# Kernel tuning notes

Measured on AMD Instinct MI355X. Metric: run time of the kernel, lower is better.

## Reference

```python
import jax, jax.numpy as jnp
import numpy as np

B, R, D, P = 32, 512, 256, 5532  # images, rois/image, feat dim, num_pids
NEG_INF = -1e30

def setup_inputs() -> dict:
    key = jax.random.key(0)
    k1, k2, k3 = jax.random.split(key, 3)
    inputs = jax.random.normal(k1, (B * R, D), dtype=jnp.float32)
    cls_scores = jax.random.uniform(k2, (B * R, 1), dtype=jnp.float32)
    roi_label = jax.random.randint(k3, (B, R), 0, P + 1)  # 0 = background -> label -1
    return {"inputs": inputs, "cls_scores": cls_scores, "roi_label": roi_label}

def reference(inputs, cls_scores, roi_label):
    x = (inputs * cls_scores).reshape(B, R, D)          # scale features by cls score
    label = roi_label - 1                               # [B,R], -1 = background
    valid = label >= 0                                  # keep labeled ROIs only
    lbl = jnp.where(valid, label, 0)

    # per-image per-pid mean prototypes via one segmented reduction
    seg = (jnp.arange(B)[:, None] * P + lbl).reshape(-1)             # [B*R]
    w = valid.reshape(-1).astype(x.dtype)
    sums = jax.ops.segment_sum(x.reshape(-1, D) * w[:, None], seg, num_segments=B * P)
    counts = jax.ops.segment_sum(w, seg, num_segments=B * P)          # [B*P]
    proto = sums / jnp.maximum(counts, 1.0)[:, None]
    proto = proto / jnp.maximum(jnp.linalg.norm(proto, axis=-1, keepdims=True), 1e-12)
    proto = jax.lax.stop_gradient(proto).reshape(B, P, D)            # .detach() in torch
    present = (counts > 0).reshape(B, P)                              # unique labels per image

    # project each ROI feature onto its image's prototypes
    logits = jnp.einsum('brd,bpd->brp', x, proto)                     # [B,R,P]
    logits = jnp.where(present[:, None, :], logits, NEG_INF)          # softmax over unique labels only
    logp = jax.nn.log_softmax(logits, axis=-1)
    nll = -jnp.take_along_axis(logp, lbl[..., None], axis=-1)[..., 0] # [B,R]
    nll = jnp.where(valid, nll, 0.0)
    n_valid = jnp.maximum(jnp.sum(valid).astype(x.dtype), 1.0)
    return jnp.sum(nll) / n_valid
```

## Files before the change

### kernel.cpp

```cpp
#include <hip/hip_runtime.h>
#include <math.h>

#define Bn 32
#define Rn 512
#define Dn 256
#define Pn 5532
#define MAXU 512

#define TRr 32
#define TCc 128
#define KCs 64
#define NSTG (Dn / KCs)
#define NBLK ((Rn / TRr) * Bn)

#define PBF_OFF    0
#define PBF_WORDS  (Bn*MAXU*Dn/2)
#define LBLC_OFF   (PBF_OFF + PBF_WORDS)
#define NUNIQ_OFF  (LBLC_OFF + Bn*Rn)
#define NVALID_OFF (NUNIQ_OFF + 32)
#define NLL_OFF    (NVALID_OFF + 32)
#define TICK_OFF   (NLL_OFF + 1)

typedef short short8 __attribute__((ext_vector_type(8)));
typedef short short4v __attribute__((ext_vector_type(4)));
typedef float floatx4 __attribute__((ext_vector_type(4)));

__device__ __forceinline__ unsigned short bf16r(float f) {
    union { float f; unsigned int u; } c; c.f = f;
    return (unsigned short)((c.u + 0x7FFFu + ((c.u >> 16) & 1u)) >> 16);
}
__device__ __forceinline__ float bfu2f(unsigned int hi16) {
    union { unsigned int u; float f; } c; c.u = hi16;
    return c.f;
}

__device__ __forceinline__ void async16(void* lds, const void* g) {
    auto* l3 = reinterpret_cast<__attribute__((address_space(3))) unsigned int*>(
                   reinterpret_cast<size_t>(lds));
    auto* g1 = reinterpret_cast<const __attribute__((address_space(1))) unsigned int*>(
                   reinterpret_cast<size_t>(g));
    __builtin_amdgcn_global_load_lds(g1, l3, 16, 0, 0);
}

__global__ __launch_bounds__(1024) void k12_prep_proto(
    const float* __restrict__ inputs, const float* __restrict__ cls,
    const int* __restrict__ roi_label,
    unsigned short* __restrict__ pbf, int* __restrict__ lblc_arr,
    int* __restrict__ nuniq, int* __restrict__ nvalid_arr,
    int* __restrict__ zwords)
{
    __shared__ int cnt_lds[Pn];
    __shared__ int cmap_lds[Pn];
    __shared__ int curs_lds[MAXU];
    __shared__ int scnt_lds[MAXU];
    __shared__ int rl_lds[Rn];
    __shared__ int wpres[16], wcnt[16];

    const int b = blockIdx.x;
    const int t = threadIdx.x;
    const int lane = t & 63, wid = t >> 6;

    if (b == 0 && t == 0) { zwords[0] = 0; zwords[1] = 0; }

    for (int i = t; i < Pn; i += 1024) cnt_lds[i] = 0;
    __syncthreads();
    int mylbl = -1;
    if (t < Rn) {
        mylbl = roi_label[b * Rn + t] - 1;
        if (mylbl >= 0) atomicAdd(&cnt_lds[mylbl], 1);
    }
    __syncthreads();

    int basePres = 0, baseCnt = 0;
    for (int i0 = 0; i0 < Pn; i0 += 1024) {
        int i = i0 + t;
        int cnt = (i < Pn) ? cnt_lds[i] : 0;
        bool pres = cnt > 0;
        unsigned long long mask = __ballot(pres);
        int pfx_pres = __popcll(mask & ((1ULL << lane) - 1ULL));
        int v = cnt;
        #pragma unroll
        for (int off = 1; off < 64; off <<= 1) {
            int u = __shfl_up(v, off);
            if (lane >= off) v += u;
        }
        int pfx_cnt = v - cnt;
        if (lane == 63) { wpres[wid] = __popcll(mask); wcnt[wid] = v; }
        __syncthreads();
        int woffP = 0, totP = 0, woffC = 0, totC = 0;
        #pragma unroll
        for (int w = 0; w < 16; ++w) {
            int p = wpres[w], c = wcnt[w];
            if (w < wid) { woffP += p; woffC += c; }
            totP += p; totC += c;
        }
        if (pres) {
            int c = basePres + woffP + pfx_pres;
            cmap_lds[i] = c;
            scnt_lds[c] = cnt;
            curs_lds[c] = baseCnt + woffC + pfx_cnt;
        }
        basePres += totP; baseCnt += totC;
        __syncthreads();
    }
    if (t < Rn) {
        int lc = (mylbl >= 0) ? cmap_lds[mylbl] : -1;
        lblc_arr[b * Rn + t] = lc;
        if (lc >= 0) {
            int pos = atomicAdd(&curs_lds[lc], 1);
            rl_lds[pos] = t;
        }
    }
    if (t == 0) { nuniq[b] = basePres; nvalid_arr[b] = baseCnt; }
    __syncthreads();
    const int U = basePres;

    for (int cb = wid; cb < U; cb += 64) {
        int cntj[4], stj[4];
        #pragma unroll
        for (int j = 0; j < 4; ++j) {
            int c = cb + 16 * j;
            bool ok = c < U;
            int cnt = ok ? scnt_lds[c] : 0;
            cntj[j] = cnt;
            stj[j]  = ok ? (curs_lds[c] - cnt) : 0;
        }
        int rj[4];
        #pragma unroll
        for (int j = 0; j < 4; ++j) rj[j] = cntj[j] ? rl_lds[stj[j]] : 0;
        float cwj[4]; float4 vj[4];
        #pragma unroll
        for (int j = 0; j < 4; ++j) {
            int row = b * Rn + rj[j];
            cwj[j] = cls[row];
            vj[j]  = *(const float4*)&inputs[(size_t)row * Dn + lane * 4];
        }
        #pragma unroll
        for (int j = 0; j < 4; ++j) {
            if (!cntj[j]) continue;
            float a0 = bfu2f(((unsigned)bf16r(vj[j].x * cwj[j])) << 16);
            float a1 = bfu2f(((unsigned)bf16r(vj[j].y * cwj[j])) << 16);
            float a2 = bfu2f(((unsigned)bf16r(vj[j].z * cwj[j])) << 16);
            float a3 = bfu2f(((unsigned)bf16r(vj[j].w * cwj[j])) << 16);
            for (int k = 1; k < cntj[j]; ++k) {
                int row = b * Rn + rl_lds[stj[j] + k];
                float cw = cls[row];
                float4 v = *(const float4*)&inputs[(size_t)row * Dn + lane * 4];
                a0 += bfu2f(((unsigned)bf16r(v.x * cw)) << 16);
                a1 += bfu2f(((unsigned)bf16r(v.y * cw)) << 16);
                a2 += bfu2f(((unsigned)bf16r(v.z * cw)) << 16);
                a3 += bfu2f(((unsigned)bf16r(v.w * cw)) << 16);
            }
            float inv = 1.0f / (float)cntj[j];
            a0 *= inv; a1 *= inv; a2 *= inv; a3 *= inv;
            float ss = a0*a0 + a1*a1 + a2*a2 + a3*a3;
            #pragma unroll
            for (int off = 32; off > 0; off >>= 1) ss += __shfl_xor(ss, off);
            float sc = 1.0f / fmaxf(sqrtf(ss), 1e-12f);
            short4v o;
            o[0] = (short)bf16r(a0 * sc); o[1] = (short)bf16r(a1 * sc);
            o[2] = (short)bf16r(a2 * sc); o[3] = (short)bf16r(a3 * sc);
            int s = b * MAXU + cb + 16 * j;
            *(short4v*)&pbf[(size_t)s * Dn + lane * 4] = o;
        }
    }
}

__global__ __launch_bounds__(256, 2) void k3_loss(
    const float* __restrict__ inputs, const float* __restrict__ cls,
    const unsigned short* __restrict__ pbf,
    const int* __restrict__ lblc_arr, const int* __restrict__ nuniq,
    const int* __restrict__ nvalid_arr,
    float* __restrict__ nll, int* __restrict__ tick, float* __restrict__ out)
{
    __shared__ __align__(16) unsigned short xs[TRr * Dn];
    __shared__ __align__(16) unsigned short psb[2][TCc * KCs];
    __shared__ int lblc[TRr];
    __shared__ float es_l[4][TRr];
    __shared__ float ds_l[4][TRr];

    const int t = threadIdx.x;
    const int lane = t & 63, w = t >> 6;
    const int q = lane >> 4, r15 = lane & 15;
    const int rt = blockIdx.x;
    const int b  = blockIdx.y;
    const int roiBase = rt * TRr;
    const int U = nuniq[b];
    const int nch = (U <= 0) ? 1 : ((U + TCc - 1) >> 7);

    if (t < TRr) lblc[t] = lblc_arr[b * Rn + roiBase + t];

#define ISSUE_PS(PC, ST, BUF)                                                \
    do {                                                                     \
        _Pragma("unroll")                                                    \
        for (int i_ = 0; i_ < 4; ++i_) {                                     \
            int ci_ = i_ * 256 + w * 64 + lane;                              \
            int pr_ = ci_ >> 3, gp_ = ci_ & 7;                               \
            int g_ = gp_ ^ (pr_ & 7);                                        \
            async16(&psb[BUF][(i_ * 256 + w * 64) * 8],                      \
                    pbf + (size_t)(b * MAXU + (PC) * TCc + pr_) * Dn         \
                        + (ST) * KCs + g_ * 8);                              \
        }                                                                    \
    } while (0)

    ISSUE_PS(0, 0, 0);

    {
        const int row = t >> 3, seg = t & 7;
        const size_t gbase = (size_t)(b * Rn + roiBase + row) * Dn + seg * 32;
        const float cw = cls[b * Rn + roiBase + row];
        #pragma unroll
        for (int jj = 0; jj < 4; ++jj) {
            float4 v0 = *(const float4*)&inputs[gbase + jj * 8];
            float4 v1 = *(const float4*)&inputs[gbase + jj * 8 + 4];
            short8 o;
            o[0] = (short)bf16r(v0.x * cw); o[1] = (short)bf16r(v0.y * cw);
            o[2] = (short)bf16r(v0.z * cw); o[3] = (short)bf16r(v0.w * cw);
            o[4] = (short)bf16r(v1.x * cw); o[5] = (short)bf16r(v1.y * cw);
            o[6] = (short)bf16r(v1.z * cw); o[7] = (short)bf16r(v1.w * cw);
            int gpos = (seg * 4 + jj) ^ (row & 7);
            *(short8*)&xs[row * Dn + gpos * 8] = o;
        }
    }
    __syncthreads();

    short8 areg[2][8];
    #pragma unroll
    for (int mt = 0; mt < 2; ++mt)
        #pragma unroll
        for (int kcs = 0; kcs < 8; ++kcs) {
            int row = mt * 16 + r15;
            int gpos = (kcs * 4 + q) ^ (row & 7);
            areg[mt][kcs] = *(const short8*)&xs[row * Dn + gpos * 8];
        }

    int lcr[2][4];
    float esum[2][4], dsum[2][4];
    #pragma unroll
    for (int mt = 0; mt < 2; ++mt)
        #pragma unroll
        for (int reg = 0; reg < 4; ++reg) {
            lcr[mt][reg] = lblc[mt * 16 + q * 4 + reg];
            esum[mt][reg] = 0.f; dsum[mt][reg] = 0.f;
        }

    for (int pc = 0; pc < nch; ++pc) {
        floatx4 acc[2][2];
        #pragma unroll
        for (int mt = 0; mt < 2; ++mt) {
            acc[mt][0] = (floatx4)0.f; acc[mt][1] = (floatx4)0.f;
        }

        #pragma unroll
        for (int st = 0; st < NSTG; ++st) {
            const int cur = st & 1;
            __syncthreads();
            int ns = pc * NSTG + st + 1;
            if (ns < nch * NSTG) ISSUE_PS(ns >> 2, ns & 3, cur ^ 1);
            #pragma unroll
            for (int kk = 0; kk < 2; ++kk) {
                short8 bb[2];
                #pragma unroll
                for (int nt = 0; nt < 2; ++nt) {
                    int r = w * 32 + nt * 16 + r15;
                    int gpos = (kk * 4 + q) ^ (r & 7);
                    bb[nt] = *(const short8*)&psb[cur][r * KCs + gpos * 8];
                }
                #pragma unroll
                for (int mt = 0; mt < 2; ++mt) {
                    acc[mt][0] = __builtin_amdgcn_mfma_f32_16x16x32_bf16(
                        areg[mt][st * 2 + kk], bb[0], acc[mt][0], 0, 0, 0);
                    acc[mt][1] = __builtin_amdgcn_mfma_f32_16x16x32_bf16(
                        areg[mt][st * 2 + kk], bb[1], acc[mt][1], 0, 0, 0);
                }
            }
        }

        #pragma unroll
        for (int nt = 0; nt < 2; ++nt) {
            int c = pc * TCc + w * 32 + nt * 16 + r15;
            bool v = c < U;
            #pragma unroll
            for (int mt = 0; mt < 2; ++mt)
                #pragma unroll
                for (int reg = 0; reg < 4; ++reg) {
                    float d = acc[mt][nt][reg];
                    if (v) esum[mt][reg] += __expf(d);
                    if (c == lcr[mt][reg]) dsum[mt][reg] += d;
                }
        }
    }
#undef ISSUE_PS

    #pragma unroll
    for (int mt = 0; mt < 2; ++mt)
        #pragma unroll
        for (int reg = 0; reg < 4; ++reg) {
            float e = esum[mt][reg], d = dsum[mt][reg];
            #pragma unroll
            for (int off = 1; off < 16; off <<= 1) {
                e += __shfl_xor(e, off);
                d += __shfl_xor(d, off);
            }
            if (r15 == 0) {
                int row = mt * 16 + q * 4 + reg;
                es_l[w][row] = e;
                ds_l[w][row] = d;
            }
        }
    __syncthreads();
    if (t < TRr) {
        float es = es_l[0][t] + es_l[1][t] + es_l[2][t] + es_l[3][t];
        float ds = ds_l[0][t] + ds_l[1][t] + ds_l[2][t] + ds_l[3][t];
        float val = (lblc[t] >= 0) ? (__logf(es) - ds) : 0.f;
        #pragma unroll
        for (int off = 1; off < 32; off <<= 1) val += __shfl_xor(val, off);
        if (t == 0) {
            atomicAdd(nll, val);
            __threadfence();
            int old = atomicAdd(tick, 1);
            if (old == NBLK - 1) {
                float total = atomicAdd(nll, 0.0f);
                int nv = 0;
                #pragma unroll
                for (int i = 0; i < Bn / 4; ++i) {
                    int4 vv = ((const int4*)nvalid_arr)[i];
                    nv += vv.x + vv.y + vv.z + vv.w;
                }
                out[0] = total / fmaxf((float)nv, 1.0f);
            }
        }
    }
}

extern "C" void kernel_launch(void* const* d_in, const int* in_sizes, int n_in,
                              void* d_out, int out_size, void* d_ws, size_t ws_size,
                              hipStream_t stream) {
    const float* inputs = (const float*)d_in[0];
    const float* cls    = (const float*)d_in[1];
    const int*   roi    = (const int*)d_in[2];
    int* wsi   = (int*)d_ws;
    float* out = (float*)d_out;

    unsigned short* pbf = (unsigned short*)(wsi + PBF_OFF);
    int*   lblc   = wsi + LBLC_OFF;
    int*   nuniq  = wsi + NUNIQ_OFF;
    int*   nvalid = wsi + NVALID_OFF;
    float* nll    = (float*)(wsi + NLL_OFF);
    int*   tick   = wsi + TICK_OFF;

    k12_prep_proto<<<Bn, 1024, 0, stream>>>(inputs, cls, roi, pbf, lblc,
                                            nuniq, nvalid, wsi + NLL_OFF);
    dim3 g(Rn / TRr, Bn);
    k3_loss<<<g, 256, 0, stream>>>(inputs, cls, pbf, lblc, nuniq, nvalid,
                                   nll, tick, out);
}
```

Baseline: 126.8 us.

## Split prototype construction into separate widely parallel kernel

The fused compaction-plus-prototype kernel ran on only 32 blocks (one per image), so the gather-and-normalise prototype work used a small fraction of the GPU. Compaction now writes per-class counts, cursors and ROI lists to global workspace. A new kernel then launches one wavefront per (image, class) slot across 4096 blocks to build the normalised bf16 prototypes. This adds a kernel launch and extra global round-trips for the compaction metadata in exchange for much more parallelism.

```diff
diff --git a/kernel.cpp b/kernel.cpp
--- a/kernel.cpp
+++ b/kernel.cpp
@@ -16,7 +16,10 @@
 #define PBF_OFF    0
 #define PBF_WORDS  (Bn*MAXU*Dn/2)
 #define LBLC_OFF   (PBF_OFF + PBF_WORDS)
-#define NUNIQ_OFF  (LBLC_OFF + Bn*Rn)
+#define CCNT_OFF   (LBLC_OFF + Bn*Rn)
+#define CURS_OFF   (CCNT_OFF + Bn*MAXU)
+#define RLIST_OFF  (CURS_OFF + Bn*MAXU)
+#define NUNIQ_OFF  (RLIST_OFF + Bn*Rn)
 #define NVALID_OFF (NUNIQ_OFF + 32)
 #define NLL_OFF    (NVALID_OFF + 32)
 #define TICK_OFF   (NLL_OFF + 1)
@@ -42,18 +45,15 @@
     __builtin_amdgcn_global_load_lds(g1, l3, 16, 0, 0);
 }
 
-__global__ __launch_bounds__(1024) void k12_prep_proto(
-    const float* __restrict__ inputs, const float* __restrict__ cls,
+__global__ __launch_bounds__(1024) void k1_compact(
     const int* __restrict__ roi_label,
-    unsigned short* __restrict__ pbf, int* __restrict__ lblc_arr,
-    int* __restrict__ nuniq, int* __restrict__ nvalid_arr,
+    int* __restrict__ lblc_arr, int* __restrict__ ccnt, int* __restrict__ cursor,
+    int* __restrict__ rlist, int* __restrict__ nuniq, int* __restrict__ nvalid_arr,
     int* __restrict__ zwords)
 {
     __shared__ int cnt_lds[Pn];
     __shared__ int cmap_lds[Pn];
     __shared__ int curs_lds[MAXU];
-    __shared__ int scnt_lds[MAXU];
-    __shared__ int rl_lds[Rn];
     __shared__ int wpres[16], wcnt[16];
 
     const int b = blockIdx.x;
@@ -97,7 +97,7 @@
         if (pres) {
             int c = basePres + woffP + pfx_pres;
             cmap_lds[i] = c;
-            scnt_lds[c] = cnt;
+            ccnt[b * MAXU + c] = cnt;
             curs_lds[c] = baseCnt + woffC + pfx_cnt;
         }
         basePres += totP; baseCnt += totC;
@@ -108,62 +108,48 @@
         lblc_arr[b * Rn + t] = lc;
         if (lc >= 0) {
             int pos = atomicAdd(&curs_lds[lc], 1);
-            rl_lds[pos] = t;
-        }
-    }
+            rlist[b * Rn + pos] = t;
+        }
+    }
+    __syncthreads();
+    if (t < MAXU && t < basePres)
+        cursor[b * MAXU + t] = curs_lds[t];
     if (t == 0) { nuniq[b] = basePres; nvalid_arr[b] = baseCnt; }
-    __syncthreads();
-    const int U = basePres;
-
-    for (int cb = wid; cb < U; cb += 64) {
-        int cntj[4], stj[4];
-        #pragma unroll
-        for (int j = 0; j < 4; ++j) {
-            int c = cb + 16 * j;
-            bool ok = c < U;
-            int cnt = ok ? scnt_lds[c] : 0;
-            cntj[j] = cnt;
-            stj[j]  = ok ? (curs_lds[c] - cnt) : 0;
-        }
-        int rj[4];
-        #pragma unroll
-        for (int j = 0; j < 4; ++j) rj[j] = cntj[j] ? rl_lds[stj[j]] : 0;
-        float cwj[4]; float4 vj[4];
-        #pragma unroll
-        for (int j = 0; j < 4; ++j) {
-            int row = b * Rn + rj[j];
-            cwj[j] = cls[row];
-            vj[j]  = *(const float4*)&inputs[(size_t)row * Dn + lane * 4];
-        }
-        #pragma unroll
-        for (int j = 0; j < 4; ++j) {
-            if (!cntj[j]) continue;
-            float a0 = bfu2f(((unsigned)bf16r(vj[j].x * cwj[j])) << 16);
-            float a1 = bfu2f(((unsigned)bf16r(vj[j].y * cwj[j])) << 16);
-            float a2 = bfu2f(((unsigned)bf16r(vj[j].z * cwj[j])) << 16);
-            float a3 = bfu2f(((unsigned)bf16r(vj[j].w * cwj[j])) << 16);
-            for (int k = 1; k < cntj[j]; ++k) {
-                int row = b * Rn + rl_lds[stj[j] + k];
-                float cw = cls[row];
-                float4 v = *(const float4*)&inputs[(size_t)row * Dn + lane * 4];
-                a0 += bfu2f(((unsigned)bf16r(v.x * cw)) << 16);
-                a1 += bfu2f(((unsigned)bf16r(v.y * cw)) << 16);
-                a2 += bfu2f(((unsigned)bf16r(v.z * cw)) << 16);
-                a3 += bfu2f(((unsigned)bf16r(v.w * cw)) << 16);
-            }
-            float inv = 1.0f / (float)cntj[j];
-            a0 *= inv; a1 *= inv; a2 *= inv; a3 *= inv;
-            float ss = a0*a0 + a1*a1 + a2*a2 + a3*a3;
-            #pragma unroll
-            for (int off = 32; off > 0; off >>= 1) ss += __shfl_xor(ss, off);
-            float sc = 1.0f / fmaxf(sqrtf(ss), 1e-12f);
-            short4v o;
-            o[0] = (short)bf16r(a0 * sc); o[1] = (short)bf16r(a1 * sc);
-            o[2] = (short)bf16r(a2 * sc); o[3] = (short)bf16r(a3 * sc);
-            int s = b * MAXU + cb + 16 * j;
-            *(short4v*)&pbf[(size_t)s * Dn + lane * 4] = o;
-        }
-    }
+}
+
+__global__ __launch_bounds__(256) void k2_proto(
+    const float* __restrict__ inputs, const float* __restrict__ cls,
+    const int* __restrict__ nuniq, const int* __restrict__ ccnt,
+    const int* __restrict__ cursor, const int* __restrict__ rlist,
+    unsigned short* __restrict__ pbf)
+{
+    const int lane = threadIdx.x & 63, wv = threadIdx.x >> 6;
+    int s = blockIdx.x * 4 + wv;
+    int b = s >> 9;
+    int c = s & (MAXU - 1);
+    if (c >= nuniq[b]) return;
+    int cnt = ccnt[s];
+    int start = cursor[s] - cnt;
+    float a0 = 0.f, a1 = 0.f, a2 = 0.f, a3 = 0.f;
+    for (int k = 0; k < cnt; ++k) {
+        int row = b * Rn + rlist[b * Rn + start + k];
+        float cw = cls[row];
+        float4 v = *(const float4*)&inputs[(size_t)row * Dn + lane * 4];
+        a0 += bfu2f(((unsigned)bf16r(v.x * cw)) << 16);
+        a1 += bfu2f(((unsigned)bf16r(v.y * cw)) << 16);
+        a2 += bfu2f(((unsigned)bf16r(v.z * cw)) << 16);
+        a3 += bfu2f(((unsigned)bf16r(v.w * cw)) << 16);
+    }
+    float inv = 1.0f / (float)cnt;
+    a0 *= inv; a1 *= inv; a2 *= inv; a3 *= inv;
+    float ss = a0*a0 + a1*a1 + a2*a2 + a3*a3;
+    #pragma unroll
+    for (int off = 32; off > 0; off >>= 1) ss += __shfl_xor(ss, off);
+    float sc = 1.0f / fmaxf(sqrtf(ss), 1e-12f);
+    short4v o;
+    o[0] = (short)bf16r(a0 * sc); o[1] = (short)bf16r(a1 * sc);
+    o[2] = (short)bf16r(a2 * sc); o[3] = (short)bf16r(a3 * sc);
+    *(short4v*)&pbf[(size_t)s * Dn + lane * 4] = o;
 }
 
 __global__ __launch_bounds__(256, 2) void k3_loss(
@@ -344,13 +330,18 @@
 
     unsigned short* pbf = (unsigned short*)(wsi + PBF_OFF);
     int*   lblc   = wsi + LBLC_OFF;
+    int*   ccnt   = wsi + CCNT_OFF;
+    int*   cursor = wsi + CURS_OFF;
+    int*   rlist  = wsi + RLIST_OFF;
     int*   nuniq  = wsi + NUNIQ_OFF;
     int*   nvalid = wsi + NVALID_OFF;
     float* nll    = (float*)(wsi + NLL_OFF);
     int*   tick   = wsi + TICK_OFF;
 
-    k12_prep_proto<<<Bn, 1024, 0, stream>>>(inputs, cls, roi, pbf, lblc,
-                                            nuniq, nvalid, wsi + NLL_OFF);
+    k1_compact<<<Bn, 1024, 0, stream>>>(roi, lblc, ccnt, cursor, rlist,
+                                        nuniq, nvalid, wsi + NLL_OFF);
+    k2_proto<<<(Bn * MAXU) / 4, 256, 0, stream>>>(inputs, cls, nuniq, ccnt,
+                                                  cursor, rlist, pbf);
     dim3 g(Rn / TRr, Bn);
     k3_loss<<<g, 256, 0, stream>>>(inputs, cls, pbf, lblc, nuniq, nvalid,
                                    nll, tick, out);
```

After: 107.4 us. -15.3%, faster.
